# Kernel optimization log

Hardware: AMD Instinct MI355X
Metric: run time of the kernel (lower is better)

Reference implementation:

```python
import jax, jax.numpy as jnp
import numpy as np

NEG_SLOPE = 0.2


def gat_conv(x, W, att_s, att_d, bias, src, dst, heads, out_c, concat):
    n = x.shape[0]
    h = (x @ W).reshape(n, heads, out_c)                      # [N,H,C]
    a_s = (h * att_s).sum(-1)                                 # [N,H]
    a_d = (h * att_d).sum(-1)                                 # [N,H]
    logits = jax.nn.leaky_relu(a_s[src] + a_d[dst], NEG_SLOPE)  # [E,H]
    # segment softmax over incoming edges of each dst node (per head)
    m = jax.ops.segment_max(logits, dst, num_segments=n)
    e = jnp.exp(logits - m[dst])
    denom = jax.ops.segment_sum(e, dst, num_segments=n)
    alpha = e / denom[dst]                                    # [E,H]
    msg = h[src] * alpha[:, :, None]                          # [E,H,C]
    out = jax.ops.segment_sum(msg, dst, num_segments=n)       # [N,H,C]
    out = out.reshape(n, heads * out_c) if concat else out.mean(axis=1)
    return out + bias


def setup_inputs() -> dict:
    key = jax.random.key(0)
    ks = jax.random.split(key, 9)
    N, IN, OUT, E = 100000, 256, 40, 1600000
    return {
        "x": jax.random.normal(ks[0], (N, IN), jnp.float32),
        "edge_index": jax.random.randint(ks[1], (2, E), 0, N, jnp.int32),
        "W1": jax.random.normal(ks[2], (IN, 64), jnp.float32) * (1.0 / np.sqrt(IN)),
        "att_src1": jax.random.normal(ks[3], (8, 8), jnp.float32) * 0.1,
        "att_dst1": jax.random.normal(ks[4], (8, 8), jnp.float32) * 0.1,
        "b1": jnp.zeros((64,), jnp.float32),
        "W2": jax.random.normal(ks[5], (64, OUT), jnp.float32) * (1.0 / 8.0),
        "att_src2": jax.random.normal(ks[6], (1, OUT), jnp.float32) * 0.1,
        "att_dst2": jax.random.normal(ks[7], (1, OUT), jnp.float32) * 0.1,
        "b2": jnp.zeros((OUT,), jnp.float32),
    }


def reference(x, edge_index, W1, att_src1, att_dst1, b1, W2, att_src2, att_dst2, b2):
    n = x.shape[0]
    loop = jnp.arange(n, dtype=edge_index.dtype)
    src = jnp.concatenate([edge_index[0], loop])  # self-loops (PyG default)
    dst = jnp.concatenate([edge_index[1], loop])
    h = gat_conv(x, W1, att_src1, att_dst1, b1, src, dst, heads=8, out_c=8, concat=True)
    h = jax.nn.relu(h)
    out = gat_conv(h, W2, att_src2, att_dst2, b2, src, dst, heads=1, out_c=W2.shape[1], concat=True)
    return jax.nn.log_softmax(out, axis=1)
```

## Files before the change

kernel.cpp:

```cpp
#include <hip/hip_runtime.h>


#define L_IN   256
#define L_C1   64
#define L_H1   8
#define L_OUT  40
#define BCAP   5120

typedef __attribute__((ext_vector_type(8))) short short8;
typedef __attribute__((ext_vector_type(4))) float f32x4;

__device__ __forceinline__ float leaky(float x){ return fmaxf(x, 0.2f*x); }
__device__ __forceinline__ unsigned f2bf(float f){
  unsigned u = __float_as_uint(f);
  return (u + 0x7fffu + ((u >> 16) & 1u)) >> 16;
}
__device__ __forceinline__ float bflo(unsigned u){ return __uint_as_float(u << 16); }
__device__ __forceinline__ float bfhi(unsigned u){ return __uint_as_float(u & 0xffff0000u); }

__global__ __launch_bounds__(256) void prep_w1(const float* __restrict__ W1,
                                               ushort* __restrict__ wt,
                                               int* __restrict__ gcur, int NB){
  const int t = threadIdx.x;
  if (blockIdx.x == 4){
    for (int i = t; i < NB; i += 256) gcur[i] = 0;
    return;
  }
  __shared__ float ws[64][65];
  const int kb = blockIdx.x;
  #pragma unroll
  for (int i = 0; i < 16; ++i){
    int idx = t + i*256;
    ws[idx >> 6][idx & 63] = W1[(size_t)(kb*64 + (idx >> 6))*64 + (idx & 63)];
  }
  __syncthreads();
  int c  = t >> 2;
  int j0 = (t & 3) * 16;
  ushort tmp[16];
  #pragma unroll
  for (int j = 0; j < 16; ++j) tmp[j] = (ushort)f2bf(ws[j0 + j][c]);
  uint4* dst = (uint4*)(wt + (size_t)c*256 + kb*64 + j0);
  dst[0] = *(uint4*)&tmp[0];
  dst[1] = *(uint4*)&tmp[8];
}

__global__ __launch_bounds__(256) void scatter_gemm1(
    const int* __restrict__ esrc, const int* __restrict__ edst,
    int* __restrict__ gcur, unsigned* __restrict__ binned, int E, int NB, int NSC,
    const float* __restrict__ x, const ushort* __restrict__ wt,
    const float* __restrict__ atts, const float* __restrict__ attd,
    ushort* __restrict__ h1b, float* __restrict__ as1, float* __restrict__ ad1, int n)
{
  __shared__ __align__(16) char smem[44032];
  const int t = threadIdx.x;

  if ((int)blockIdx.x < NSC){
    int* hist  = (int*)smem;
    int* rbase = hist + 512;
    int* cur   = rbase + 512;
    const int e0 = blockIdx.x * 4096;
    hist[t] = 0; hist[t+256] = 0; cur[t] = 0; cur[t+256] = 0;
    __syncthreads();
    int sv[16], dv[16];
    const bool full = (e0 + 4096 <= E);
    if (full){
      #pragma unroll
      for (int j = 0; j < 4; ++j){
        int p4 = (e0 >> 2) + j*256 + t;
        int4 s4 = ((const int4*)esrc)[p4];
        int4 d4 = ((const int4*)edst)[p4];
        sv[4*j+0]=s4.x; sv[4*j+1]=s4.y; sv[4*j+2]=s4.z; sv[4*j+3]=s4.w;
        dv[4*j+0]=d4.x; dv[4*j+1]=d4.y; dv[4*j+2]=d4.z; dv[4*j+3]=d4.w;
        atomicAdd(&hist[d4.x >> 8], 1); atomicAdd(&hist[d4.y >> 8], 1);
        atomicAdd(&hist[d4.z >> 8], 1); atomicAdd(&hist[d4.w >> 8], 1);
      }
    } else {
      #pragma unroll
      for (int j = 0; j < 16; ++j){
        int idx = e0 + j*256 + t;
        if (idx < E){
          sv[j] = esrc[idx]; dv[j] = edst[idx];
          atomicAdd(&hist[dv[j] >> 8], 1);
        } else dv[j] = -1;
      }
    }
    __syncthreads();
    if (hist[t])                   rbase[t]     = atomicAdd(&gcur[t],     hist[t]);
    if (t+256 < NB && hist[t+256]) rbase[t+256] = atomicAdd(&gcur[t+256], hist[t+256]);
    __syncthreads();
    #pragma unroll
    for (int j = 0; j < 16; ++j){
      if (dv[j] >= 0){
        int b = dv[j] >> 8;
        int off = rbase[b] + atomicAdd(&cur[b], 1);
        if (off < BCAP)
          binned[(size_t)b*BCAP + off] =
            (unsigned)sv[j] | ((unsigned)(dv[j] & 255) << 17);
      }
    }
    return;
  }

  ushort (*xs)[136] = (ushort(*)[136])(smem);
  ushort (*ws)[136] = (ushort(*)[136])(smem + 17408);
  ushort (*hs)[72]  = (ushort(*)[72]) (smem + 34816);
  const int rb = (blockIdx.x - NSC) * 64;
  const int wv = t >> 6;
  const int ln = t & 63;
  const int fr = ln & 15;
  const int fq = ln >> 4;

  f32x4 acc[4];
  #pragma unroll
  for (int cb = 0; cb < 4; ++cb) acc[cb] = (f32x4){0.f,0.f,0.f,0.f};

  for (int kb = 0; kb < 2; ++kb){
    if (kb) __syncthreads();
    #pragma unroll
    for (int i = 0; i < 8; ++i){
      int idx = t + i*256;
      int row = idx >> 5, c4 = idx & 31;
      float4 v = make_float4(0.f,0.f,0.f,0.f);
      if (rb + row < n) v = *(const float4*)(x + (size_t)(rb+row)*L_IN + kb*128 + c4*4);
      uint2 p;
      p.x = f2bf(v.x) | (f2bf(v.y) << 16);
      p.y = f2bf(v.z) | (f2bf(v.w) << 16);
      *(uint2*)&xs[row][c4*4] = p;
    }
    #pragma unroll
    for (int i = 0; i < 4; ++i){
      int idx = t + i*256;
      int row = idx >> 4, c8 = idx & 15;
      *(uint4*)&ws[row][c8*8] = *(const uint4*)(wt + (size_t)row*256 + kb*128 + c8*8);
    }
    __syncthreads();
    #pragma unroll
    for (int ks = 0; ks < 4; ++ks){
      short8 a = *(const short8*)&xs[wv*16 + fr][ks*32 + fq*8];
      #pragma unroll
      for (int cb = 0; cb < 4; ++cb){
        short8 b = *(const short8*)&ws[cb*16 + fr][ks*32 + fq*8];
        acc[cb] = __builtin_amdgcn_mfma_f32_16x16x32_bf16(a, b, acc[cb], 0, 0, 0);
      }
    }
  }
  __syncthreads();
  #pragma unroll
  for (int cb = 0; cb < 4; ++cb)
    #pragma unroll
    for (int r = 0; r < 4; ++r)
      hs[wv*16 + fq*4 + r][cb*16 + fr] = (ushort)f2bf(acc[cb][r]);
  __syncthreads();
  #pragma unroll
  for (int p = 0; p < 2; ++p){
    int pid = t + p*256;
    int row = pid >> 3, hd = pid & 7;
    if (rb + row < n){
      uint4 u = *(const uint4*)&hs[row][hd*8];
      float v0=bflo(u.x), v1=bfhi(u.x), v2=bflo(u.y), v3=bfhi(u.y);
      float v4=bflo(u.z), v5=bfhi(u.z), v6=bflo(u.w), v7=bfhi(u.w);
      const float* sa = atts + hd*8;
      const float* da = attd + hd*8;
      float ds = v0*sa[0]+v1*sa[1]+v2*sa[2]+v3*sa[3]+v4*sa[4]+v5*sa[5]+v6*sa[6]+v7*sa[7];
      float dd = v0*da[0]+v1*da[1]+v2*da[2]+v3*da[3]+v4*da[4]+v5*da[5]+v6*da[6]+v7*da[7];
      as1[(size_t)(rb+row)*L_H1 + hd] = ds;
      ad1[(size_t)(rb+row)*L_H1 + hd] = dd;
    }
  }
  #pragma unroll
  for (int i = 0; i < 2; ++i){
    int idx = t + i*256;
    int row = idx >> 3, c8 = idx & 7;
    if (rb + row < n)
      *(uint4*)(h1b + (size_t)(rb+row)*L_C1 + c8*8) = *(const uint4*)&hs[row][c8*8];
  }
}

__global__ __launch_bounds__(256) void bucket_csr(const unsigned* __restrict__ binned,
    const int* __restrict__ gcur, int2* __restrict__ nodeptr, int* __restrict__ csr,
    int N){
  __shared__ unsigned ebuf[BCAP];
  __shared__ int cnt[256], pref[256], cur[256];
  const int t = threadIdx.x;
  const int b = blockIdx.x;
  int ne = gcur[b]; if (ne > BCAP) ne = BCAP;
  const int base = b * BCAP;
  cnt[t] = 0; cur[t] = 0;
  __syncthreads();
  for (int i = t; i < ne; i += 256){
    unsigned e = binned[base + i];
    ebuf[i] = e;
    atomicAdd(&cnt[(e >> 17) & 255u], 1);
  }
  __syncthreads();
  pref[t] = cnt[t];
  __syncthreads();
  for (int off = 1; off < 256; off <<= 1){
    int a = (t >= off) ? pref[t-off] : 0;
    __syncthreads();
    pref[t] += a;
    __syncthreads();
  }
  int excl = pref[t] - cnt[t];
  __syncthreads();
  pref[t] = excl;
  int d = (b << 8) + t;
  if (d < N) nodeptr[d] = make_int2(base + excl, cnt[t]);
  __syncthreads();
  for (int i = t; i < ne; i += 256){
    unsigned e = ebuf[i];
    int ln = (int)((e >> 17) & 255u);
    int pos = base + pref[ln] + atomicAdd(&cur[ln], 1);
    csr[pos] = (int)(e & 0x1FFFFu);
  }
}

__global__ __launch_bounds__(256) void agg1_kernel(
    const int2* __restrict__ nodeptr, const int* __restrict__ csr,
    const ushort* __restrict__ h1b, const float* __restrict__ as1,
    const float* __restrict__ ad1, const float* __restrict__ b1,
    ushort* __restrict__ hrb, int n)
{
  int wid  = (blockIdx.x*blockDim.x + threadIdx.x) >> 6;
  int lane = threadIdx.x & 63;
  if (wid >= n) return;
  int2 np  = nodeptr[wid];
  int beg  = np.x;
  int degt = np.y + 1;

  const int h  = lane & 7;
  const int eg = lane >> 3;
  const int cp = lane & 31;
  const int ep = lane >> 5;
  const int hc = cp >> 2;

  float adn = ad1[(size_t)wid*L_H1 + h];
  float ax = 0.f, ay = 0.f, sp = 0.f;

  #define A1_GRP_W(g, SRCV, WV)                                            \
    { int i_ = (g)*8 + eg;                                                 \
      SRCV = (i_ < degt-1) ? csr[beg + i_] : wid;                          \
      float l_ = (i_ < degt) ? leaky(as1[(size_t)SRCV*L_H1 + h] + adn)     \
                             : -1e30f;                                     \
      WV = __expf(l_); sp += WV; }
  #define A1_GRP_G(SRCV, WV)                                               \
    _Pragma("unroll")                                                      \
    for (int e0 = 0; e0 < 8; e0 += 2){                                     \
      int e_  = e0 + ep;                                                   \
      float we_ = __shfl(WV,   e_*8 + hc);                                 \
      int   se_ = __shfl(SRCV, e_*8);                                      \
      unsigned u_ = *(const unsigned*)(h1b + (size_t)se_*L_C1 + cp*2);     \
      ax += we_ * bflo(u_);                                                \
      ay += we_ * bfhi(u_);                                                \
    }

  if (degt <= 16){
    int s0, s1; float w0, w1;
    A1_GRP_W(0, s0, w0) A1_GRP_W(1, s1, w1)
    A1_GRP_G(s0, w0) A1_GRP_G(s1, w1)
  } else if (degt <= 24){
    int s0, s1, s2; float w0, w1, w2;
    A1_GRP_W(0, s0, w0) A1_GRP_W(1, s1, w1) A1_GRP_W(2, s2, w2)
    A1_GRP_G(s0, w0) A1_GRP_G(s1, w1) A1_GRP_G(s2, w2)
  } else {
    const int ngrp = (degt + 7) >> 3;
    for (int g = 0; g < ngrp; ++g){
      int sg; float wg;
      A1_GRP_W(g, sg, wg)
      A1_GRP_G(sg, wg)
    }
  }
  #undef A1_GRP_W
  #undef A1_GRP_G

  #pragma unroll
  for (int off = 8; off < 64; off <<= 1) sp += __shfl_xor(sp, off);
  float rinv = 1.0f / __shfl(sp, hc);
  ax += __shfl_xor(ax, 32);
  ay += __shfl_xor(ay, 32);
  if (lane < 32){
    float2 bv = *(const float2*)&b1[cp*2];
    float r0 = fmaxf(ax*rinv + bv.x, 0.f);
    float r1 = fmaxf(ay*rinv + bv.y, 0.f);
    *(unsigned*)(hrb + (size_t)wid*L_C1 + cp*2) = f2bf(r0) | (f2bf(r1) << 16);
  }
}

__global__ __launch_bounds__(256) void gemm2_kernel(
    const ushort* __restrict__ hrb, const float* __restrict__ W2,
    const float* __restrict__ atts2, const float* __restrict__ attd2,
    ushort* __restrict__ h2b, float* __restrict__ as2, float* __restrict__ ad2, int n)
{
  __shared__ float w2s[64*40];
  const int t = threadIdx.x;
  for (int i = t; i < 64*40; i += 256) w2s[i] = W2[i];
  __syncthreads();
  int row = blockIdx.x*256 + t;
  if (row >= n) return;

  uint4 rv[8];
  #pragma unroll
  for (int q = 0; q < 8; ++q)
    rv[q] = *(const uint4*)(hrb + (size_t)row*L_C1 + q*8);

  f32x4 acc4[10];
  #pragma unroll
  for (int j = 0; j < 10; ++j) acc4[j] = (f32x4){0.f,0.f,0.f,0.f};

  #pragma unroll
  for (int q = 0; q < 8; ++q){
    unsigned uu[4] = {rv[q].x, rv[q].y, rv[q].z, rv[q].w};
    #pragma unroll
    for (int d = 0; d < 4; ++d){
      int k = q*8 + d*2;
      float v0 = bflo(uu[d]), v1 = bfhi(uu[d]);
      const f32x4* w0 = (const f32x4*)&w2s[k*40];
      const f32x4* w1 = (const f32x4*)&w2s[(k+1)*40];
      #pragma unroll
      for (int j = 0; j < 10; ++j) acc4[j] += v0*w0[j] + v1*w1[j];
    }
  }

  float acc[40];
  #pragma unroll
  for (int j = 0; j < 10; ++j){
    acc[4*j+0]=acc4[j][0]; acc[4*j+1]=acc4[j][1];
    acc[4*j+2]=acc4[j][2]; acc[4*j+3]=acc4[j][3];
  }
  float ps = 0.f, pd = 0.f;
  #pragma unroll
  for (int j = 0; j < 40; ++j){ ps += acc[j]*atts2[j]; pd += acc[j]*attd2[j]; }
  unsigned pk[20];
  #pragma unroll
  for (int q = 0; q < 20; ++q) pk[q] = f2bf(acc[2*q]) | (f2bf(acc[2*q+1]) << 16);
  uint4* dst = (uint4*)(h2b + (size_t)row*L_OUT);
  #pragma unroll
  for (int q = 0; q < 5; ++q) dst[q] = make_uint4(pk[4*q],pk[4*q+1],pk[4*q+2],pk[4*q+3]);
  as2[row] = ps;
  ad2[row] = pd;
}

__global__ __launch_bounds__(256) void agg2_kernel(
    const int2* __restrict__ nodeptr, const int* __restrict__ csr,
    const ushort* __restrict__ h2b, const float* __restrict__ as2,
    const float* __restrict__ ad2, const float* __restrict__ b2,
    float* __restrict__ out, int n)
{
  int wid  = (blockIdx.x*blockDim.x + threadIdx.x) >> 6;
  int lane = threadIdx.x & 63;
  if (wid >= n) return;
  int2 np  = nodeptr[wid];
  int beg  = np.x;
  int degt = np.y + 1;

  const int eidx = (lane < 60) ? (lane / 20) : 0;
  const int cq   = (lane < 60) ? (lane % 20) : 0;

  float adn = ad2[wid];
  float ax = 0.f, ay = 0.f, sp = 0.f;

  #define A2_STEP(e_, SRCV, WV, CNT)                                       \
    { int ee_ = (e_);                                                      \
      int es_ = (ee_ < 64) ? ee_ : 63;                                     \
      float we_ = __shfl(WV,   es_);                                       \
      int   se_ = __shfl(SRCV, es_);                                       \
      we_ = (ee_ < (CNT)) ? we_ : 0.f;                                     \
      unsigned u_ = *(const unsigned*)(h2b + (size_t)se_*L_OUT + cq*2);    \
      ax += we_ * bflo(u_);                                                \
      ay += we_ * bfhi(u_); }

  if (degt <= 64){
    int i = lane;
    int src = (i < degt-1) ? csr[beg + i] : wid;
    float l = (i < degt) ? leaky(as2[src] + adn) : -1e30f;
    float w = __expf(l);
    sp = w;
    if (degt <= 18){
      #pragma unroll
      for (int j = 0; j < 2; ++j){
        A2_STEP(j*9 + 0*3 + eidx, src, w, degt)
        A2_STEP(j*9 + 1*3 + eidx, src, w, degt)
        A2_STEP(j*9 + 2*3 + eidx, src, w, degt)
      }
    } else if (degt <= 27){
      #pragma unroll
      for (int j = 0; j < 3; ++j){
        A2_STEP(j*9 + 0*3 + eidx, src, w, degt)
        A2_STEP(j*9 + 1*3 + eidx, src, w, degt)
        A2_STEP(j*9 + 2*3 + eidx, src, w, degt)
      }
    } else if (degt <= 36){
      #pragma unroll
      for (int j = 0; j < 4; ++j){
        A2_STEP(j*9 + 0*3 + eidx, src, w, degt)
        A2_STEP(j*9 + 1*3 + eidx, src, w, degt)
        A2_STEP(j*9 + 2*3 + eidx, src, w, degt)
      }
    } else {
      for (int e0 = 0; e0 < degt; e0 += 9){
        A2_STEP(e0 + 0*3 + eidx, src, w, degt)
        A2_STEP(e0 + 1*3 + eidx, src, w, degt)
        A2_STEP(e0 + 2*3 + eidx, src, w, degt)
      }
    }
  } else {
    const int ngrp = (degt + 63) >> 6;
    for (int g = 0; g < ngrp; ++g){
      int i = g*64 + lane;
      int src = (i < degt-1) ? csr[beg + i] : wid;
      float l = (i < degt) ? leaky(as2[src] + adn) : -1e30f;
      float w = __expf(l);
      sp += w;
      int cnt = degt - g*64; if (cnt > 64) cnt = 64;
      for (int e0 = 0; e0 < cnt; e0 += 9){
        A2_STEP(e0 + 0*3 + eidx, src, w, cnt)
        A2_STEP(e0 + 1*3 + eidx, src, w, cnt)
        A2_STEP(e0 + 2*3 + eidx, src, w, cnt)
      }
    }
  }
  #undef A2_STEP

  #pragma unroll
  for (int off = 1; off < 64; off <<= 1) sp += __shfl_xor(sp, off);
  float rinv = 1.0f / sp;

  float ax0 = __shfl(ax, cq), ax1 = __shfl(ax, cq+20), ax2 = __shfl(ax, cq+40);
  float ay0 = __shfl(ay, cq), ay1 = __shfl(ay, cq+20), ay2 = __shfl(ay, cq+40);
  float axs = (ax0 + ax1) + ax2;
  float ays = (ay0 + ay1) + ay2;

  bool act = (lane < 20);
  float o0 = axs*rinv + b2[cq*2];
  float o1 = ays*rinv + b2[cq*2+1];
  float mx = act ? fmaxf(o0, o1) : -1e30f;
  #pragma unroll
  for (int off = 1; off < 32; off <<= 1) mx = fmaxf(mx, __shfl_xor(mx, off));
  float ex = act ? (__expf(o0 - mx) + __expf(o1 - mx)) : 0.f;
  #pragma unroll
  for (int off = 1; off < 32; off <<= 1) ex += __shfl_xor(ex, off);
  float lse = mx + __logf(ex);
  if (act){
    float2 r = make_float2(o0 - lse, o1 - lse);
    *(float2*)(out + (size_t)wid*L_OUT + cq*2) = r;
  }
}

extern "C" void kernel_launch(void* const* d_in, const int* in_sizes, int n_in,
                              void* d_out, int out_size, void* d_ws, size_t ws_size,
                              hipStream_t stream)
{
  const float* x    = (const float*)d_in[0];
  const int*   ei   = (const int*)  d_in[1];
  const float* W1   = (const float*)d_in[2];
  const float* as1w = (const float*)d_in[3];
  const float* ad1w = (const float*)d_in[4];
  const float* b1   = (const float*)d_in[5];
  const float* W2   = (const float*)d_in[6];
  const float* as2w = (const float*)d_in[7];
  const float* ad2w = (const float*)d_in[8];
  const float* b2   = (const float*)d_in[9];

  const int N = in_sizes[0] / L_IN;
  const int E = in_sizes[1] / 2;
  const int NB = (N + 255) >> 8;
  const int NSC = (E + 4095) / 4096;
  const int NG1 = (N + 63) / 64;
  const int* esrc = ei;
  const int* edst = ei + E;
  float* out = (float*)d_out;

  char* w = (char*)d_ws;
  auto alloc = [&](size_t bytes)->char*{
    char* p = w; w += (bytes + 255) & ~size_t(255); return p;
  };
  ushort* h1b  = (ushort*)alloc((size_t)N*L_C1*2);
  float*  as1  = (float*) alloc((size_t)N*L_H1*4);
  float*  ad1  = (float*) alloc((size_t)N*L_H1*4);
  size_t union_sz = (size_t)N*L_C1*2 + (size_t)N*L_OUT*2;
  if (union_sz < (size_t)NB*BCAP*4) union_sz = (size_t)NB*BCAP*4;
  char*  ub    = alloc(union_sz);
  ushort* hrb  = (ushort*)ub;
  ushort* h2b  = (ushort*)(ub + (size_t)N*L_C1*2);
  unsigned* binned = (unsigned*)ub;
  float*  as2  = (float*) alloc((size_t)N*4);
  float*  ad2  = (float*) alloc((size_t)N*4);
  ushort* wt   = (ushort*)alloc((size_t)64*256*2);
  int2*  nodeptr=(int2*)  alloc((size_t)N*8);
  int*   csr   = (int*)   alloc((size_t)NB*BCAP*4);
  int*   gcur  = (int*)   alloc((size_t)NB*4);

  prep_w1     <<<5,          256, 0, stream>>>(W1, wt, gcur, NB);
  scatter_gemm1<<<NSC + NG1, 256, 0, stream>>>(esrc, edst, gcur, binned, E, NB, NSC,
                                               x, wt, as1w, ad1w, h1b, as1, ad1, N);
  bucket_csr  <<<NB,         256, 0, stream>>>(binned, gcur, nodeptr, csr, N);
  agg1_kernel <<<(N+3)/4,    256, 0, stream>>>(nodeptr, csr, h1b, as1, ad1, b1, hrb, N);
  gemm2_kernel<<<(N+255)/256,256, 0, stream>>>(hrb, W2, as2w, ad2w, h2b, as2, ad2, N);
  agg2_kernel <<<(N+3)/4,    256, 0, stream>>>(nodeptr, csr, h2b, as2, ad2, b2, out, N);
}
```

Baseline: 180.2 us.

## Split scatter/gemm1 kernel, prefetch second K half, widen bucket_csr to 512 threads

New measurement: 185.5 us. +2.9%, slower.

```diff
diff --git a/kernel.cpp b/kernel.cpp
--- a/kernel.cpp
+++ b/kernel.cpp
@@ -44,107 +44,146 @@
   dst[1] = *(uint4*)&tmp[8];
 }
 
-__global__ __launch_bounds__(256) void scatter_gemm1(
-    const int* __restrict__ esrc, const int* __restrict__ edst,
-    int* __restrict__ gcur, unsigned* __restrict__ binned, int E, int NB, int NSC,
+__global__ __launch_bounds__(256) void bin_scatter(const int* __restrict__ esrc,
+    const int* __restrict__ edst, int* __restrict__ gcur,
+    unsigned* __restrict__ binned, int E, int NB){
+  __shared__ int hist[512], rbase[512], cur[512];
+  const int t  = threadIdx.x;
+  const int e0 = blockIdx.x * 4096;
+  hist[t] = 0; hist[t+256] = 0; cur[t] = 0; cur[t+256] = 0;
+  __syncthreads();
+  int sv[16], dv[16];
+  const bool full = (e0 + 4096 <= E);
+  if (full){
+    #pragma unroll
+    for (int j = 0; j < 4; ++j){
+      int p4 = (e0 >> 2) + j*256 + t;
+      int4 s4 = ((const int4*)esrc)[p4];
+      int4 d4 = ((const int4*)edst)[p4];
+      sv[4*j+0]=s4.x; sv[4*j+1]=s4.y; sv[4*j+2]=s4.z; sv[4*j+3]=s4.w;
+      dv[4*j+0]=d4.x; dv[4*j+1]=d4.y; dv[4*j+2]=d4.z; dv[4*j+3]=d4.w;
+      atomicAdd(&hist[d4.x >> 8], 1); atomicAdd(&hist[d4.y >> 8], 1);
+      atomicAdd(&hist[d4.z >> 8], 1); atomicAdd(&hist[d4.w >> 8], 1);
+    }
+  } else {
+    #pragma unroll
+    for (int j = 0; j < 16; ++j){
+      int idx = e0 + j*256 + t;
+      if (idx < E){
+        sv[j] = esrc[idx]; dv[j] = edst[idx];
+        atomicAdd(&hist[dv[j] >> 8], 1);
+      } else dv[j] = -1;
+    }
+  }
+  __syncthreads();
+  if (hist[t])                   rbase[t]     = atomicAdd(&gcur[t],     hist[t]);
+  if (t+256 < NB && hist[t+256]) rbase[t+256] = atomicAdd(&gcur[t+256], hist[t+256]);
+  __syncthreads();
+  #pragma unroll
+  for (int j = 0; j < 16; ++j){
+    if (dv[j] >= 0){
+      int b = dv[j] >> 8;
+      int off = rbase[b] + atomicAdd(&cur[b], 1);
+      if (off < BCAP)
+        binned[(size_t)b*BCAP + off] =
+          (unsigned)sv[j] | ((unsigned)(dv[j] & 255) << 17);
+    }
+  }
+}
+
+__global__ __launch_bounds__(256) void gemm1_kernel(
     const float* __restrict__ x, const ushort* __restrict__ wt,
     const float* __restrict__ atts, const float* __restrict__ attd,
     ushort* __restrict__ h1b, float* __restrict__ as1, float* __restrict__ ad1, int n)
 {
-  __shared__ __align__(16) char smem[44032];
-  const int t = threadIdx.x;
-
-  if ((int)blockIdx.x < NSC){
-    int* hist  = (int*)smem;
-    int* rbase = hist + 512;
-    int* cur   = rbase + 512;
-    const int e0 = blockIdx.x * 4096;
-    hist[t] = 0; hist[t+256] = 0; cur[t] = 0; cur[t+256] = 0;
-    __syncthreads();
-    int sv[16], dv[16];
-    const bool full = (e0 + 4096 <= E);
-    if (full){
-      #pragma unroll
-      for (int j = 0; j < 4; ++j){
-        int p4 = (e0 >> 2) + j*256 + t;
-        int4 s4 = ((const int4*)esrc)[p4];
-        int4 d4 = ((const int4*)edst)[p4];
-        sv[4*j+0]=s4.x; sv[4*j+1]=s4.y; sv[4*j+2]=s4.z; sv[4*j+3]=s4.w;
-        dv[4*j+0]=d4.x; dv[4*j+1]=d4.y; dv[4*j+2]=d4.z; dv[4*j+3]=d4.w;
-        atomicAdd(&hist[d4.x >> 8], 1); atomicAdd(&hist[d4.y >> 8], 1);
-        atomicAdd(&hist[d4.z >> 8], 1); atomicAdd(&hist[d4.w >> 8], 1);
-      }
-    } else {
-      #pragma unroll
-      for (int j = 0; j < 16; ++j){
-        int idx = e0 + j*256 + t;
-        if (idx < E){
-          sv[j] = esrc[idx]; dv[j] = edst[idx];
-          atomicAdd(&hist[dv[j] >> 8], 1);
-        } else dv[j] = -1;
-      }
-    }
-    __syncthreads();
-    if (hist[t])                   rbase[t]     = atomicAdd(&gcur[t],     hist[t]);
-    if (t+256 < NB && hist[t+256]) rbase[t+256] = atomicAdd(&gcur[t+256], hist[t+256]);
-    __syncthreads();
-    #pragma unroll
-    for (int j = 0; j < 16; ++j){
-      if (dv[j] >= 0){
-        int b = dv[j] >> 8;
-        int off = rbase[b] + atomicAdd(&cur[b], 1);
-        if (off < BCAP)
-          binned[(size_t)b*BCAP + off] =
-            (unsigned)sv[j] | ((unsigned)(dv[j] & 255) << 17);
-      }
-    }
-    return;
-  }
-
+  __shared__ __align__(16) char smem[34816];
   ushort (*xs)[136] = (ushort(*)[136])(smem);
   ushort (*ws)[136] = (ushort(*)[136])(smem + 17408);
-  ushort (*hs)[72]  = (ushort(*)[72]) (smem + 34816);
-  const int rb = (blockIdx.x - NSC) * 64;
+  ushort (*hs)[72]  = (ushort(*)[72]) (smem);
+  const int t  = threadIdx.x;
+  const int rb = blockIdx.x * 64;
   const int wv = t >> 6;
   const int ln = t & 63;
   const int fr = ln & 15;
   const int fq = ln >> 4;
 
+  #pragma unroll
+  for (int i = 0; i < 8; ++i){
+    int idx = t + i*256;
+    int row = idx >> 5, c4 = idx & 31;
+    float4 v = make_float4(0.f,0.f,0.f,0.f);
+    if (rb + row < n) v = *(const float4*)(x + (size_t)(rb+row)*L_IN + c4*4);
+    uint2 p;
+    p.x = f2bf(v.x) | (f2bf(v.y) << 16);
+    p.y = f2bf(v.z) | (f2bf(v.w) << 16);
+    *(uint2*)&xs[row][c4*4] = p;
+  }
+  #pragma unroll
+  for (int i = 0; i < 4; ++i){
+    int idx = t + i*256;
+    int row = idx >> 4, c8 = idx & 15;
+    *(uint4*)&ws[row][c8*8] = *(const uint4*)(wt + (size_t)row*256 + c8*8);
+  }
+  __syncthreads();
+
+  float4 px[8]; uint4 pw[4];
+  #pragma unroll
+  for (int i = 0; i < 8; ++i){
+    int idx = t + i*256;
+    int row = idx >> 5, c4 = idx & 31;
+    px[i] = make_float4(0.f,0.f,0.f,0.f);
+    if (rb + row < n) px[i] = *(const float4*)(x + (size_t)(rb+row)*L_IN + 128 + c4*4);
+  }
+  #pragma unroll
+  for (int i = 0; i < 4; ++i){
+    int idx = t + i*256;
+    int row = idx >> 4, c8 = idx & 15;
+    pw[i] = *(const uint4*)(wt + (size_t)row*256 + 128 + c8*8);
+  }
+
   f32x4 acc[4];
   #pragma unroll
   for (int cb = 0; cb < 4; ++cb) acc[cb] = (f32x4){0.f,0.f,0.f,0.f};
 
-  for (int kb = 0; kb < 2; ++kb){
-    if (kb) __syncthreads();
+  #pragma unroll
+  for (int ks = 0; ks < 4; ++ks){
+    short8 a = *(const short8*)&xs[wv*16 + fr][ks*32 + fq*8];
     #pragma unroll
-    for (int i = 0; i < 8; ++i){
-      int idx = t + i*256;
-      int row = idx >> 5, c4 = idx & 31;
-      float4 v = make_float4(0.f,0.f,0.f,0.f);
-      if (rb + row < n) v = *(const float4*)(x + (size_t)(rb+row)*L_IN + kb*128 + c4*4);
-      uint2 p;
-      p.x = f2bf(v.x) | (f2bf(v.y) << 16);
-      p.y = f2bf(v.z) | (f2bf(v.w) << 16);
-      *(uint2*)&xs[row][c4*4] = p;
-    }
+    for (int cb = 0; cb < 4; ++cb){
+      short8 b = *(const short8*)&ws[cb*16 + fr][ks*32 + fq*8];
+      acc[cb] = __builtin_amdgcn_mfma_f32_16x16x32_bf16(a, b, acc[cb], 0, 0, 0);
+    }
+  }
+  __syncthreads();
+
+  #pragma unroll
+  for (int i = 0; i < 8; ++i){
+    int idx = t + i*256;
+    int row = idx >> 5, c4 = idx & 31;
+    uint2 p;
+    p.x = f2bf(px[i].x) | (f2bf(px[i].y) << 16);
+    p.y = f2bf(px[i].z) | (f2bf(px[i].w) << 16);
+    *(uint2*)&xs[row][c4*4] = p;
+  }
+  #pragma unroll
+  for (int i = 0; i < 4; ++i){
+    int idx = t + i*256;
+    int row = idx >> 4, c8 = idx & 15;
+    *(uint4*)&ws[row][c8*8] = pw[i];
+  }
+  __syncthreads();
+
+  #pragma unroll
+  for (int ks = 0; ks < 4; ++ks){
+    short8 a = *(const short8*)&xs[wv*16 + fr][ks*32 + fq*8];
     #pragma unroll
-    for (int i = 0; i < 4; ++i){
-      int idx = t + i*256;
-      int row = idx >> 4, c8 = idx & 15;
-      *(uint4*)&ws[row][c8*8] = *(const uint4*)(wt + (size_t)row*256 + kb*128 + c8*8);
-    }
-    __syncthreads();
-    #pragma unroll
-    for (int ks = 0; ks < 4; ++ks){
-      short8 a = *(const short8*)&xs[wv*16 + fr][ks*32 + fq*8];
-      #pragma unroll
-      for (int cb = 0; cb < 4; ++cb){
-        short8 b = *(const short8*)&ws[cb*16 + fr][ks*32 + fq*8];
-        acc[cb] = __builtin_amdgcn_mfma_f32_16x16x32_bf16(a, b, acc[cb], 0, 0, 0);
-      }
-    }
-  }
-  __syncthreads();
+    for (int cb = 0; cb < 4; ++cb){
+      short8 b = *(const short8*)&ws[cb*16 + fr][ks*32 + fq*8];
+      acc[cb] = __builtin_amdgcn_mfma_f32_16x16x32_bf16(a, b, acc[cb], 0, 0, 0);
+    }
+  }
+  __syncthreads();
+
   #pragma unroll
   for (int cb = 0; cb < 4; ++cb)
     #pragma unroll
@@ -176,7 +215,7 @@
   }
 }
 
-__global__ __launch_bounds__(256) void bucket_csr(const unsigned* __restrict__ binned,
+__global__ __launch_bounds__(512) void bucket_csr(const unsigned* __restrict__ binned,
     const int* __restrict__ gcur, int2* __restrict__ nodeptr, int* __restrict__ csr,
     int N){
   __shared__ unsigned ebuf[BCAP];
@@ -185,29 +224,33 @@
   const int b = blockIdx.x;
   int ne = gcur[b]; if (ne > BCAP) ne = BCAP;
   const int base = b * BCAP;
-  cnt[t] = 0; cur[t] = 0;
-  __syncthreads();
-  for (int i = t; i < ne; i += 256){
+  if (t < 256){ cnt[t] = 0; cur[t] = 0; }
+  __syncthreads();
+  for (int i = t; i < ne; i += 512){
     unsigned e = binned[base + i];
     ebuf[i] = e;
     atomicAdd(&cnt[(e >> 17) & 255u], 1);
   }
   __syncthreads();
-  pref[t] = cnt[t];
+  if (t < 256) pref[t] = cnt[t];
   __syncthreads();
   for (int off = 1; off < 256; off <<= 1){
-    int a = (t >= off) ? pref[t-off] : 0;
+    int a = 0;
+    if (t < 256 && t >= off) a = pref[t-off];
     __syncthreads();
-    pref[t] += a;
+    if (t < 256) pref[t] += a;
     __syncthreads();
   }
-  int excl = pref[t] - cnt[t];
-  __syncthreads();
-  pref[t] = excl;
-  int d = (b << 8) + t;
-  if (d < N) nodeptr[d] = make_int2(base + excl, cnt[t]);
-  __syncthreads();
-  for (int i = t; i < ne; i += 256){
+  int excl = 0;
+  if (t < 256) excl = pref[t] - cnt[t];
+  __syncthreads();
+  if (t < 256){
+    pref[t] = excl;
+    int d = (b << 8) + t;
+    if (d < N) nodeptr[d] = make_int2(base + excl, cnt[t]);
+  }
+  __syncthreads();
+  for (int i = t; i < ne; i += 512){
     unsigned e = ebuf[i];
     int ln = (int)((e >> 17) & 255u);
     int pos = base + pref[ln] + atomicAdd(&cur[ln], 1);
@@ -465,7 +508,6 @@
   const int E = in_sizes[1] / 2;
   const int NB = (N + 255) >> 8;
   const int NSC = (E + 4095) / 4096;
-  const int NG1 = (N + 63) / 64;
   const int* esrc = ei;
   const int* edst = ei + E;
   float* out = (float*)d_out;
@@ -491,9 +533,9 @@
   int*   gcur  = (int*)   alloc((size_t)NB*4);
 
   prep_w1     <<<5,          256, 0, stream>>>(W1, wt, gcur, NB);
-  scatter_gemm1<<<NSC + NG1, 256, 0, stream>>>(esrc, edst, gcur, binned, E, NB, NSC,
-                                               x, wt, as1w, ad1w, h1b, as1, ad1, N);
-  bucket_csr  <<<NB,         256, 0, stream>>>(binned, gcur, nodeptr, csr, N);
+  bin_scatter <<<NSC,        256, 0, stream>>>(esrc, edst, gcur, binned, E, NB);
+  gemm1_kernel<<<(N+63)/64,  256, 0, stream>>>(x, wt, as1w, ad1w, h1b, as1, ad1, N);
+  bucket_csr  <<<NB,         512, 0, stream>>>(binned, gcur, nodeptr, csr, N);
   agg1_kernel <<<(N+3)/4,    256, 0, stream>>>(nodeptr, csr, h1b, as1, ad1, b1, hrb, N);
   gemm2_kernel<<<(N+255)/256,256, 0, stream>>>(hrb, W2, as2w, ad2w, h2b, as2, ad2, N);
   agg2_kernel <<<(N+3)/4,    256, 0, stream>>>(nodeptr, csr, h2b, as2, ad2, b2, out, N);
```
